# Performance work log

Measured on AMD Instinct MI355X. Metric: run time of the kernel, lower is better.

Reference implementation:

```python
import jax, jax.numpy as jnp
import numpy as np

NNZ_A = 2_000_000
NNZ_B = 2_000_000
TAR_NNZ = 2_000_000
M = 4_000_000  # number of multiply (gather) pairs in the acd descriptor
D = 32         # hidden feature dim


def setup_inputs() -> dict:
    key = jax.random.key(0)
    k1, k2, k3, k4, k5 = jax.random.split(key, 5)
    Aval = jax.random.normal(k1, (NNZ_A, D), dtype=jnp.float32)
    Bval = jax.random.normal(k2, (NNZ_B, D), dtype=jnp.float32)
    # acd descriptor: row 0 -> target output nnz index, row 1 -> A nnz index, row 2 -> B nnz index
    a = jax.random.randint(k3, (M,), 0, TAR_NNZ)
    c = jax.random.randint(k4, (M,), 0, NNZ_A)
    d = jax.random.randint(k5, (M,), 0, NNZ_B)
    acd = jnp.stack([a, c, d], axis=0).astype(jnp.int64)
    return {"Aval": Aval, "Bval": Bval, "acd": acd, "tar_nnz": TAR_NNZ}


def reference(Aval, Bval, acd, tar_nnz):
    # spspmm with precomputed acd: gather aligned nnz values, multiply, scatter-sum
    # msg: (M, D)
    msg = Aval[acd[1]] * Bval[acd[2]]
    # aggr='sum' -> segment sum into target sparse tensor values (tar_nnz, D)
    out = jax.ops.segment_sum(msg, acd[0], num_segments=tar_nnz)
    return out
```

## Files before the change

kernel.cpp:

```cpp
#include <hip/hip_runtime.h>


#define FEAT_D 32
#define BUCKET_BITS 8
#define BUCKET_ROWS (1 << BUCKET_BITS)
#define ROW_STRIDE 33
#define MAX_BINS 8192
#define SCAN_PER (MAX_BINS / 1024)

typedef unsigned int u32;
typedef unsigned long long u64;

__global__ __launch_bounds__(256) void hist_kernel(
    const int* __restrict__ acd, u32* __restrict__ ghist, int M, int NB)
{
    __shared__ u32 lh[MAX_BINS];
    for (int i = threadIdx.x; i < NB; i += blockDim.x) lh[i] = 0;
    __syncthreads();
    int stride = gridDim.x * blockDim.x;
    for (int i = blockIdx.x * blockDim.x + threadIdx.x; i < M; i += stride) {
        int a = acd[i];
        atomicAdd(&lh[a >> BUCKET_BITS], 1u);
    }
    __syncthreads();
    for (int i = threadIdx.x; i < NB; i += blockDim.x)
        if (lh[i]) atomicAdd(&ghist[i], lh[i]);
}

__global__ __launch_bounds__(1024) void scan_kernel(
    const u32* __restrict__ ghist, u32* __restrict__ offsets,
    u32* __restrict__ cursors, int NB)
{
    __shared__ u32 partial[1024];
    int t = threadIdx.x;
    u32 v[SCAN_PER];
    u32 sum = 0;
    for (int k = 0; k < SCAN_PER; k++) {
        int i = t * SCAN_PER + k;
        v[k] = (i < NB) ? ghist[i] : 0u;
        sum += v[k];
    }
    partial[t] = sum;
    __syncthreads();
    for (int off = 1; off < 1024; off <<= 1) {
        u32 mine = partial[t];
        u32 add = (t >= off) ? partial[t - off] : 0u;
        __syncthreads();
        partial[t] = mine + add;
        __syncthreads();
    }
    u32 running = (t == 0) ? 0u : partial[t - 1];
    for (int k = 0; k < SCAN_PER; k++) {
        int i = t * SCAN_PER + k;
        if (i < NB) {
            offsets[i] = running;
            cursors[i] = running;
        }
        running += v[k];
    }
    if (t == 0) offsets[NB] = partial[1023];
}

__global__ __launch_bounds__(256) void scatter_kernel(
    const int* __restrict__ acd, u32* __restrict__ cursors,
    u64* __restrict__ rec, int M)
{
    int stride = gridDim.x * blockDim.x;
    for (int i = blockIdx.x * blockDim.x + threadIdx.x; i < M; i += stride) {
        u32 a = (u32)acd[i];
        u32 c = (u32)acd[M + i];
        u32 d = (u32)acd[2 * M + i];
        u32 b = a >> BUCKET_BITS;
        u32 pos = atomicAdd(&cursors[b], 1u);
        rec[pos] = ((u64)d << 32) | (u64)(c | ((a & (BUCKET_ROWS - 1)) << 21));
    }
}

__global__ __launch_bounds__(512) void accum_kernel(
    const u64* __restrict__ rec, const u32* __restrict__ offsets,
    const float* __restrict__ Aval, const float* __restrict__ Bval,
    float* __restrict__ out, int tar)
{
    __shared__ float acc[BUCKET_ROWS * ROW_STRIDE];
    int t = threadIdx.x;
    int b = blockIdx.x;
    for (int i = t; i < BUCKET_ROWS * ROW_STRIDE; i += 512) acc[i] = 0.f;
    __syncthreads();

    u32 s = offsets[b], e = offsets[b + 1];
    int g  = t >> 3;
    int f4 = t & 7;

    u32 idx = s + (u32)g;
    if (idx < e) {
        u64 r = __builtin_nontemporal_load(rec + idx);
        u32 w0 = (u32)r;
        u32 d  = (u32)(r >> 32);
        u32 c  = w0 & 0x1FFFFFu;
        u32 al = (w0 >> 21) & (BUCKET_ROWS - 1);
        float4 av = *reinterpret_cast<const float4*>(Aval + (size_t)c * FEAT_D + f4 * 4);
        float4 bv = *reinterpret_cast<const float4*>(Bval + (size_t)d * FEAT_D + f4 * 4);

        for (u32 nxt = idx + 64; nxt < e; nxt += 64) {
            u64 r2 = __builtin_nontemporal_load(rec + nxt);
            u32 w02 = (u32)r2;
            u32 d2  = (u32)(r2 >> 32);
            u32 c2  = w02 & 0x1FFFFFu;
            u32 al2 = (w02 >> 21) & (BUCKET_ROWS - 1);
            float4 av2 = *reinterpret_cast<const float4*>(Aval + (size_t)c2 * FEAT_D + f4 * 4);
            float4 bv2 = *reinterpret_cast<const float4*>(Bval + (size_t)d2 * FEAT_D + f4 * 4);

            float* p = &acc[al * ROW_STRIDE + f4 * 4];
            atomicAdd(p + 0, av.x * bv.x);
            atomicAdd(p + 1, av.y * bv.y);
            atomicAdd(p + 2, av.z * bv.z);
            atomicAdd(p + 3, av.w * bv.w);

            av = av2; bv = bv2; al = al2;
        }
        float* p = &acc[al * ROW_STRIDE + f4 * 4];
        atomicAdd(p + 0, av.x * bv.x);
        atomicAdd(p + 1, av.y * bv.y);
        atomicAdd(p + 2, av.z * bv.z);
        atomicAdd(p + 3, av.w * bv.w);
    }
    __syncthreads();

    int row0 = b << BUCKET_BITS;
    int nrows = tar - row0;
    if (nrows > BUCKET_ROWS) nrows = BUCKET_ROWS;
    int nel = nrows * FEAT_D;
    float* obase = out + (size_t)row0 * FEAT_D;
    for (int i = t; i < nel; i += 512) {
        int row = i >> 5, col = i & 31;
        __builtin_nontemporal_store(acc[row * ROW_STRIDE + col], obase + i);
    }
}

__global__ __launch_bounds__(256) void spspmm_scatter_kernel(
    const float* __restrict__ Aval, const float* __restrict__ Bval,
    const int* __restrict__ acd, float* __restrict__ out, int M)
{
    int gid = blockIdx.x * blockDim.x + threadIdx.x;
    int pair = gid >> 3;
    int f4 = gid & 7;
    if (pair >= M) return;
    int a = acd[pair];
    int c = acd[M + pair];
    int d = acd[2 * M + pair];
    const float4 av = *reinterpret_cast<const float4*>(Aval + (size_t)c * FEAT_D + f4 * 4);
    const float4 bv = *reinterpret_cast<const float4*>(Bval + (size_t)d * FEAT_D + f4 * 4);
    float* o = out + (size_t)a * FEAT_D + f4 * 4;
    atomicAdd(o + 0, av.x * bv.x);
    atomicAdd(o + 1, av.y * bv.y);
    atomicAdd(o + 2, av.z * bv.z);
    atomicAdd(o + 3, av.w * bv.w);
}

extern "C" void kernel_launch(void* const* d_in, const int* in_sizes, int n_in,
                              void* d_out, int out_size, void* d_ws, size_t ws_size,
                              hipStream_t stream) {
    const float* Aval = (const float*)d_in[0];
    const float* Bval = (const float*)d_in[1];
    const int*   acd  = (const int*)d_in[2];
    float*       out  = (float*)d_out;

    const int M   = in_sizes[2] / 3;
    const int tar = out_size / FEAT_D;
    const int NB  = (tar + BUCKET_ROWS - 1) >> BUCKET_BITS;

    size_t rec_bytes = (size_t)M * sizeof(u64);
    size_t need = rec_bytes + (size_t)(3 * NB + 2) * sizeof(u32) + 256;

    if (NB <= MAX_BINS && ws_size >= need) {
        u64* rec     = (u64*)d_ws;
        u32* ghist   = (u32*)((char*)d_ws + rec_bytes);
        u32* offsets = ghist + NB;
        u32* cursors = offsets + (NB + 1);

        hipMemsetAsync(ghist, 0, (size_t)NB * sizeof(u32), stream);
        hist_kernel<<<1024, 256, 0, stream>>>(acd, ghist, M, NB);
        scan_kernel<<<1, 1024, 0, stream>>>(ghist, offsets, cursors, NB);
        scatter_kernel<<<2048, 256, 0, stream>>>(acd, cursors, rec, M);
        accum_kernel<<<NB, 512, 0, stream>>>(rec, offsets, Aval, Bval, out, tar);
    } else {
        hipMemsetAsync(d_out, 0, (size_t)out_size * sizeof(float), stream);
        const long long total_threads = (long long)M * 8;
        const long long grid = (total_threads + 255) / 256;
        spspmm_scatter_kernel<<<dim3((unsigned)grid), dim3(256), 0, stream>>>(
            Aval, Bval, acd, out, M);
    }
}
```

Baseline: 1.307 ms.

## Replace single-pass bucket scatter with two-level coarse/fine radix partition

Splits the record scatter into two passes. A coarse pass buffers records per 64-bucket group in shared memory and flushes them in contiguous chunks. A fine pass then redistributes each group into its final buckets using shared-memory cursors. This replaces the random global atomics and scattered 8-byte writes across about 7800 buckets with mostly coalesced writes, at the cost of an extra full read and write of the record array and a second workspace buffer. The accum kernel also drops its nontemporal loads and masks the packed fine-bucket bits out of d.

```diff
diff --git a/kernel.cpp b/kernel.cpp
--- a/kernel.cpp
+++ b/kernel.cpp
@@ -7,6 +7,9 @@
 #define ROW_STRIDE 33
 #define MAX_BINS 8192
 #define SCAN_PER (MAX_BINS / 1024)
+#define COARSE_SHIFT 14
+#define NBC_MAX 128
+#define CBUF 64
 
 typedef unsigned int u32;
 typedef unsigned long long u64;
@@ -29,7 +32,7 @@
 
 __global__ __launch_bounds__(1024) void scan_kernel(
     const u32* __restrict__ ghist, u32* __restrict__ offsets,
-    u32* __restrict__ cursors, int NB)
+    u32* __restrict__ cursors, u32* __restrict__ ccursor, int NB, int NBC)
 {
     __shared__ u32 partial[1024];
     int t = threadIdx.x;
@@ -59,6 +62,145 @@
         running += v[k];
     }
     if (t == 0) offsets[NB] = partial[1023];
+    __syncthreads();
+    if (t < NBC) {
+        int fi = t << 6;
+        if (fi > NB) fi = NB;
+        ccursor[t] = offsets[fi];
+    }
+}
+
+__global__ __launch_bounds__(512) void scatter_coarse(
+    const int* __restrict__ acd, u32* __restrict__ ccursor,
+    u64* __restrict__ crec, int M, int NBC)
+{
+    __shared__ u64 buf[NBC_MAX * CBUF];
+    __shared__ u32 cnt[NBC_MAX];
+    __shared__ u32 base[NBC_MAX];
+    int t = threadIdx.x;
+    const int R = 4096;
+    int nrounds = (M + R - 1) / R;
+    for (int rd = blockIdx.x; rd < nrounds; rd += gridDim.x) {
+        int lo = rd * R;
+        int hi = lo + R; if (hi > M) hi = M;
+        for (int i = t; i < NBC_MAX; i += 512) cnt[i] = 0;
+        __syncthreads();
+        for (int i = lo + t; i < hi; i += 512) {
+            u32 a = (u32)acd[i];
+            u32 c = (u32)acd[M + i];
+            u32 d = (u32)acd[2 * M + i];
+            u32 fl = (a >> BUCKET_BITS) & 63u;
+            u64 r = ((u64)(d | (fl << 21)) << 32)
+                  | (u64)(c | ((a & (u32)(BUCKET_ROWS - 1)) << 21));
+            u32 cb = a >> COARSE_SHIFT;
+            u32 slot = atomicAdd(&cnt[cb], 1u);
+            if (slot < (u32)CBUF) {
+                buf[(cb << 6) + slot] = r;
+            } else {
+                u32 pos = atomicAdd(&ccursor[cb], 1u);
+                crec[pos] = r;
+            }
+        }
+        __syncthreads();
+        for (int i = t; i < NBC; i += 512) {
+            u32 n = cnt[i]; if (n > (u32)CBUF) n = (u32)CBUF;
+            base[i] = n ? atomicAdd(&ccursor[i], n) : 0u;
+        }
+        __syncthreads();
+        for (int i = t; i < (NBC << 6); i += 512) {
+            int b = i >> 6, j = i & (CBUF - 1);
+            u32 n = cnt[b]; if (n > (u32)CBUF) n = (u32)CBUF;
+            if ((u32)j < n) crec[base[b] + j] = buf[i];
+        }
+        __syncthreads();
+    }
+}
+
+__global__ __launch_bounds__(512) void scatter_fine(
+    const u64* __restrict__ crec, const u32* __restrict__ offsets,
+    u64* __restrict__ rec, int NB)
+{
+    __shared__ u32 fcur[64];
+    int cb = blockIdx.x;
+    int t = threadIdx.x;
+    int f0 = cb << 6;
+    int f1 = f0 + 64; if (f1 > NB) f1 = NB;
+    u32 s = offsets[f0];
+    u32 e = offsets[f1];
+    if (t < 64) {
+        int fi = f0 + t; if (fi > NB) fi = NB;
+        fcur[t] = offsets[fi];
+    }
+    __syncthreads();
+    for (u32 i = s + (u32)t; i < e; i += 512) {
+        u64 r = crec[i];
+        u32 fl = (u32)(r >> 53) & 63u;
+        u32 pos = atomicAdd(&fcur[fl], 1u);
+        u32 w0 = (u32)r;
+        u32 d21 = (u32)(r >> 32) & 0x1FFFFFu;
+        rec[pos] = ((u64)d21 << 32) | (u64)w0;
+    }
+}
+
+__global__ __launch_bounds__(512) void accum_kernel(
+    const u64* __restrict__ rec, const u32* __restrict__ offsets,
+    const float* __restrict__ Aval, const float* __restrict__ Bval,
+    float* __restrict__ out, int tar)
+{
+    __shared__ float acc[BUCKET_ROWS * ROW_STRIDE];
+    int t = threadIdx.x;
+    int b = blockIdx.x;
+    for (int i = t; i < BUCKET_ROWS * ROW_STRIDE; i += 512) acc[i] = 0.f;
+    __syncthreads();
+
+    u32 s = offsets[b], e = offsets[b + 1];
+    int g  = t >> 3;
+    int f4 = t & 7;
+
+    u32 idx = s + (u32)g;
+    if (idx < e) {
+        u64 r = rec[idx];
+        u32 w0 = (u32)r;
+        u32 d  = (u32)(r >> 32) & 0x1FFFFFu;
+        u32 c  = w0 & 0x1FFFFFu;
+        u32 al = (w0 >> 21) & (BUCKET_ROWS - 1);
+        float4 av = *reinterpret_cast<const float4*>(Aval + (size_t)c * FEAT_D + f4 * 4);
+        float4 bv = *reinterpret_cast<const float4*>(Bval + (size_t)d * FEAT_D + f4 * 4);
+
+        for (u32 nxt = idx + 64; nxt < e; nxt += 64) {
+            u64 r2 = rec[nxt];
+            u32 w02 = (u32)r2;
+            u32 d2  = (u32)(r2 >> 32) & 0x1FFFFFu;
+            u32 c2  = w02 & 0x1FFFFFu;
+            u32 al2 = (w02 >> 21) & (BUCKET_ROWS - 1);
+            float4 av2 = *reinterpret_cast<const float4*>(Aval + (size_t)c2 * FEAT_D + f4 * 4);
+            float4 bv2 = *reinterpret_cast<const float4*>(Bval + (size_t)d2 * FEAT_D + f4 * 4);
+
+            float* p = &acc[al * ROW_STRIDE + f4 * 4];
+            atomicAdd(p + 0, av.x * bv.x);
+            atomicAdd(p + 1, av.y * bv.y);
+            atomicAdd(p + 2, av.z * bv.z);
+            atomicAdd(p + 3, av.w * bv.w);
+
+            av = av2; bv = bv2; al = al2;
+        }
+        float* p = &acc[al * ROW_STRIDE + f4 * 4];
+        atomicAdd(p + 0, av.x * bv.x);
+        atomicAdd(p + 1, av.y * bv.y);
+        atomicAdd(p + 2, av.z * bv.z);
+        atomicAdd(p + 3, av.w * bv.w);
+    }
+    __syncthreads();
+
+    int row0 = b << BUCKET_BITS;
+    int nrows = tar - row0;
+    if (nrows > BUCKET_ROWS) nrows = BUCKET_ROWS;
+    int nel = nrows * FEAT_D;
+    float* obase = out + (size_t)row0 * FEAT_D;
+    for (int i = t; i < nel; i += 512) {
+        int row = i >> 5, col = i & 31;
+        __builtin_nontemporal_store(acc[row * ROW_STRIDE + col], obase + i);
+    }
 }
 
 __global__ __launch_bounds__(256) void scatter_kernel(
@@ -73,67 +215,6 @@
         u32 b = a >> BUCKET_BITS;
         u32 pos = atomicAdd(&cursors[b], 1u);
         rec[pos] = ((u64)d << 32) | (u64)(c | ((a & (BUCKET_ROWS - 1)) << 21));
-    }
-}
-
-__global__ __launch_bounds__(512) void accum_kernel(
-    const u64* __restrict__ rec, const u32* __restrict__ offsets,
-    const float* __restrict__ Aval, const float* __restrict__ Bval,
-    float* __restrict__ out, int tar)
-{
-    __shared__ float acc[BUCKET_ROWS * ROW_STRIDE];
-    int t = threadIdx.x;
-    int b = blockIdx.x;
-    for (int i = t; i < BUCKET_ROWS * ROW_STRIDE; i += 512) acc[i] = 0.f;
-    __syncthreads();
-
-    u32 s = offsets[b], e = offsets[b + 1];
-    int g  = t >> 3;
-    int f4 = t & 7;
-
-    u32 idx = s + (u32)g;
-    if (idx < e) {
-        u64 r = __builtin_nontemporal_load(rec + idx);
-        u32 w0 = (u32)r;
-        u32 d  = (u32)(r >> 32);
-        u32 c  = w0 & 0x1FFFFFu;
-        u32 al = (w0 >> 21) & (BUCKET_ROWS - 1);
-        float4 av = *reinterpret_cast<const float4*>(Aval + (size_t)c * FEAT_D + f4 * 4);
-        float4 bv = *reinterpret_cast<const float4*>(Bval + (size_t)d * FEAT_D + f4 * 4);
-
-        for (u32 nxt = idx + 64; nxt < e; nxt += 64) {
-            u64 r2 = __builtin_nontemporal_load(rec + nxt);
-            u32 w02 = (u32)r2;
-            u32 d2  = (u32)(r2 >> 32);
-            u32 c2  = w02 & 0x1FFFFFu;
-            u32 al2 = (w02 >> 21) & (BUCKET_ROWS - 1);
-            float4 av2 = *reinterpret_cast<const float4*>(Aval + (size_t)c2 * FEAT_D + f4 * 4);
-            float4 bv2 = *reinterpret_cast<const float4*>(Bval + (size_t)d2 * FEAT_D + f4 * 4);
-
-            float* p = &acc[al * ROW_STRIDE + f4 * 4];
-            atomicAdd(p + 0, av.x * bv.x);
-            atomicAdd(p + 1, av.y * bv.y);
-            atomicAdd(p + 2, av.z * bv.z);
-            atomicAdd(p + 3, av.w * bv.w);
-
-            av = av2; bv = bv2; al = al2;
-        }
-        float* p = &acc[al * ROW_STRIDE + f4 * 4];
-        atomicAdd(p + 0, av.x * bv.x);
-        atomicAdd(p + 1, av.y * bv.y);
-        atomicAdd(p + 2, av.z * bv.z);
-        atomicAdd(p + 3, av.w * bv.w);
-    }
-    __syncthreads();
-
-    int row0 = b << BUCKET_BITS;
-    int nrows = tar - row0;
-    if (nrows > BUCKET_ROWS) nrows = BUCKET_ROWS;
-    int nel = nrows * FEAT_D;
-    float* obase = out + (size_t)row0 * FEAT_D;
-    for (int i = t; i < nel; i += 512) {
-        int row = i >> 5, col = i & 31;
-        __builtin_nontemporal_store(acc[row * ROW_STRIDE + col], obase + i);
     }
 }
 
@@ -168,19 +249,37 @@
     const int M   = in_sizes[2] / 3;
     const int tar = out_size / FEAT_D;
     const int NB  = (tar + BUCKET_ROWS - 1) >> BUCKET_BITS;
+    const int NBC = (NB + 63) >> 6;
 
     size_t rec_bytes = (size_t)M * sizeof(u64);
-    size_t need = rec_bytes + (size_t)(3 * NB + 2) * sizeof(u32) + 256;
-
-    if (NB <= MAX_BINS && ws_size >= need) {
+    size_t small = (size_t)(3 * NB + 2 + NBC) * sizeof(u32) + 256;
+    size_t need2 = 2 * rec_bytes + small;
+    size_t need1 = rec_bytes + small;
+
+    if (NB <= MAX_BINS && NBC <= NBC_MAX && ws_size >= need2) {
+        u64* crec    = (u64*)d_ws;
+        u64* rec     = (u64*)((char*)d_ws + rec_bytes);
+        u32* ghist   = (u32*)((char*)d_ws + 2 * rec_bytes);
+        u32* offsets = ghist + NB;
+        u32* cursors = offsets + (NB + 1);
+        u32* ccursor = cursors + NB;
+
+        hipMemsetAsync(ghist, 0, (size_t)NB * sizeof(u32), stream);
+        hist_kernel<<<1024, 256, 0, stream>>>(acd, ghist, M, NB);
+        scan_kernel<<<1, 1024, 0, stream>>>(ghist, offsets, cursors, ccursor, NB, NBC);
+        scatter_coarse<<<512, 512, 0, stream>>>(acd, ccursor, crec, M, NBC);
+        scatter_fine<<<NBC, 512, 0, stream>>>(crec, offsets, rec, NB);
+        accum_kernel<<<NB, 512, 0, stream>>>(rec, offsets, Aval, Bval, out, tar);
+    } else if (NB <= MAX_BINS && ws_size >= need1) {
         u64* rec     = (u64*)d_ws;
         u32* ghist   = (u32*)((char*)d_ws + rec_bytes);
         u32* offsets = ghist + NB;
         u32* cursors = offsets + (NB + 1);
+        u32* ccursor = cursors + NB;
 
         hipMemsetAsync(ghist, 0, (size_t)NB * sizeof(u32), stream);
         hist_kernel<<<1024, 256, 0, stream>>>(acd, ghist, M, NB);
-        scan_kernel<<<1, 1024, 0, stream>>>(ghist, offsets, cursors, NB);
+        scan_kernel<<<1, 1024, 0, stream>>>(ghist, offsets, cursors, ccursor, NB, NBC);
         scatter_kernel<<<2048, 256, 0, stream>>>(acd, cursors, rec, M);
         accum_kernel<<<NB, 512, 0, stream>>>(rec, offsets, Aval, Bval, out, tar);
     } else {
```

Result: faster. 1.206 ms (-7.7%).
